# Optimization experiments

Measured on AMD Instinct MI355X. Metric: run time of the kernel, lower is better.

The kernel has to match this reference:

```python
import jax, jax.numpy as jnp
import numpy as np

# Model dims: batch, seq, d_model, heads, layers, vocab, ffn, max_distance
B, S, D, H, L, V, F, M = 2, 1024, 1024, 16, 6, 32000, 4096, 1024
Dh = D // H


def setup_inputs() -> dict:
    key = jax.random.key(0)
    ks = jax.random.split(key, 24)
    std = 0.02
    w = lambda k, shape: (jax.random.normal(k, shape, jnp.float32) * std)
    return {
        "tokens": jax.random.randint(ks[0], (B, S), 0, V, jnp.int32),
        "emb": w(ks[1], (V, D)),
        "Wq": w(ks[2], (L, D, D)), "bq": jnp.zeros((L, D), jnp.float32),
        "Wk": w(ks[3], (L, D, D)), "bk": jnp.zeros((L, D), jnp.float32),
        "Wv": w(ks[4], (L, D, D)), "bv": jnp.zeros((L, D), jnp.float32),
        "Wo": w(ks[5], (L, D, D)), "bo": jnp.zeros((L, D), jnp.float32),
        "rpe": w(ks[6], (L, M, Dh)),  # per-layer key-RPE embedding table
        "ln1_s": jnp.ones((L, D), jnp.float32), "ln1_b": jnp.zeros((L, D), jnp.float32),
        "ln2_s": jnp.ones((L, D), jnp.float32), "ln2_b": jnp.zeros((L, D), jnp.float32),
        "W1": w(ks[7], (L, D, F)), "b1": jnp.zeros((L, F), jnp.float32),
        "W2": w(ks[8], (L, F, D)), "b2": jnp.zeros((L, D), jnp.float32),
        "Wout": w(ks[9], (D, V)), "bout": jnp.zeros((V,), jnp.float32),
    }


def _ln(x, s, b):
    mu = jnp.mean(x, -1, keepdims=True)
    var = jnp.mean((x - mu) ** 2, -1, keepdims=True)
    return (x - mu) * jax.lax.rsqrt(var + 1e-5) * s + b


def _forward(tokens, emb, Wq, bq, Wk, bk, Wv, bv, Wo, bo, rpe,
             ln1_s, ln1_b, ln2_s, ln2_b, W1, b1, W2, b2, Wout, bout):
    x = emb[tokens]  # (B, S, D); dropout is identity at inference
    mask = jnp.tril(jnp.ones((S, S), bool))
    inv_sqrt_d = np.float32(1.0 / np.sqrt(Dh))

    def block(x, p):
        (wq, bq_, wk, bk_, wv, bv_, wo, bo_, rp,
         l1s, l1b, l2s, l2b, w1, b1_, w2, b2_) = p
        heads = lambda W, b: (x @ W + b).reshape(B, S, H, Dh).transpose(0, 2, 1, 3)
        q, k, v = heads(wq, bq_), heads(wk, bk_), heads(wv, bv_)
        qk = jnp.einsum('bhqd,bhkd->bhqk', q, k)
        # Music-Transformer skew: srel = Q @ E^T, pad-left 1, reshape, drop first row
        srel = jnp.einsum('bhqd,md->bhqm', q, rp[-S:])  # M == S, no clipping branch
        srel = jnp.pad(srel, ((0, 0), (0, 0), (0, 0), (1, 0)))
        srel = srel.reshape(B, H, S + 1, S)[:, :, 1:, :]
        logits = (qk + srel) * inv_sqrt_d
        logits = jnp.where(mask, logits, jnp.float32(-1e9))
        wgt = jax.nn.softmax(logits, axis=-1)
        o = jnp.einsum('bhqk,bhkd->bhqd', wgt, v).transpose(0, 2, 1, 3).reshape(B, S, D)
        o = o @ wo + bo_
        x2 = _ln(x + o, l1s, l1b)           # post-LN residual (attention)
        f = jax.nn.gelu(x2 @ w1 + b1_) @ w2 + b2_
        return _ln(x2 + f, l2s, l2b), None  # post-LN residual (FFN)

    x, _ = jax.lax.scan(block, x, (Wq, bq, Wk, bk, Wv, bv, Wo, bo, rpe,
                                   ln1_s, ln1_b, ln2_s, ln2_b, W1, b1, W2, b2))
    return x @ Wout + bout  # (B, S, V)


def reference(tokens, emb, Wq, bq, Wk, bk, Wv, bv, Wo, bo, rpe,
              ln1_s, ln1_b, ln2_s, ln2_b, W1, b1, W2, b2, Wout, bout):
    return _forward(tokens, emb, Wq, bq, Wk, bk, Wv, bv, Wo, bo, rpe,
                    ln1_s, ln1_b, ln2_s, ln2_b, W1, b1, W2, b2, Wout, bout)
```

## Files before the change

kernel.cpp:

```cpp
#include <hip/hip_runtime.h>
#include <hip/hip_bf16.h>
#include <cstdint>

constexpr int NB = 2, NS = 1024, ND = 1024, NH = 16, NL = 6, NV = 32000, NF = 4096, NDH = 64;

using bf16 = __hip_bfloat16;
typedef __bf16 bf16x8 __attribute__((ext_vector_type(8)));
typedef float f32x4 __attribute__((ext_vector_type(4)));

#define AS1(p) ((const __attribute__((address_space(1))) void*)(p))
#define AS3(p) ((__attribute__((address_space(3))) void*)(p))

__device__ __forceinline__ float gelu_f(float x) {
  float z = 1.5957691216057308f * (x + 0.044715f * x * x * x);
  return x / (1.f + __expf(-z));
}

template<int EP, bool HASBIAS>
__global__ __launch_bounds__(256)
void gemm128_bt(const bf16* __restrict__ A, const bf16* __restrict__ Bt,
                void* __restrict__ Cv, const float* __restrict__ bias,
                int K, int lda, int ldb, int ldc, long sEP)
{
  const int nM = gridDim.y, nN = gridDim.x;
  const int nwg = nM * nN;
  const int bid = blockIdx.y * nN + blockIdx.x;
  const int qq = nwg >> 3;
  const int wg = (bid & 7) * qq + (bid >> 3);
  const int m0 = (wg % nM) * 128;
  const int n0 = (wg / nM) * 256;

  __shared__ char lds[73728];

  const int tid  = threadIdx.x;
  const int lane = tid & 63;
  const int wid  = tid >> 6;
  const int wn   = wid * 64;
  const int l15  = lane & 15;
  const int rdk  = ((lane >> 4) * 16) ^ ((l15 >> 3) << 5);

  const int srow = wid * 16 + (lane >> 2);
  const int scol = ((lane & 3) * 8) ^ (((lane >> 5) & 1) << 4);
  const bf16* gA = A  + (long)(m0 + srow) * lda + scol;
  const bf16* gB = Bt + (long)(n0 + srow) * ldb + scol;
  const long a64 = 64l * lda, b64 = 64l * ldb;

  f32x4 acc[8][4] = {};
  const int NT = K >> 5;

#define STG(t_, b_) do {                                                               \
    char* dA = lds + (b_) * 24576 + wid * 1024;                                        \
    char* dB = lds + (b_) * 24576 + 8192 + wid * 1024;                                 \
    const long ko_ = (long)(t_) * 32;                                                  \
    __builtin_amdgcn_global_load_lds(AS1(gA + ko_),           AS3(dA),         16, 0, 0); \
    __builtin_amdgcn_global_load_lds(AS1(gA + ko_ + a64),     AS3(dA + 4096),  16, 0, 0); \
    __builtin_amdgcn_global_load_lds(AS1(gB + ko_),           AS3(dB),         16, 0, 0); \
    __builtin_amdgcn_global_load_lds(AS1(gB + ko_ + b64),     AS3(dB + 4096),  16, 0, 0); \
    __builtin_amdgcn_global_load_lds(AS1(gB + ko_ + 2 * b64), AS3(dB + 8192),  16, 0, 0); \
    __builtin_amdgcn_global_load_lds(AS1(gB + ko_ + 3 * b64), AS3(dB + 12288), 16, 0, 0); \
  } while (0)

#define TBODY(cur_) do {                                                               \
    const char* la_ = lds + (cur_) * 24576;                                            \
    const char* lb_ = la_ + 8192;                                                      \
    bf16x8 bf_[4], af_[8];                                                             \
    _Pragma("unroll") for (int j_ = 0; j_ < 4; ++j_)                                   \
      bf_[j_] = *(const bf16x8*)(lb_ + (wn + j_ * 16 + l15) * 64 + rdk);               \
    _Pragma("unroll") for (int i_ = 0; i_ < 8; ++i_)                                   \
      af_[i_] = *(const bf16x8*)(la_ + (i_ * 16 + l15) * 64 + rdk);                    \
    __builtin_amdgcn_s_setprio(1);                                                     \
    _Pragma("unroll") for (int i_ = 0; i_ < 8; ++i_)                                   \
      _Pragma("unroll") for (int j_ = 0; j_ < 4; ++j_)                                 \
        acc[i_][j_] = __builtin_amdgcn_mfma_f32_16x16x32_bf16(af_[i_], bf_[j_], acc[i_][j_], 0, 0, 0); \
    __builtin_amdgcn_s_setprio(0);                                                     \
  } while (0)

  STG(0, 0); STG(1, 1);
  int cur = 0, nxt = 2;
  for (int t = 0; t < NT - 1; ++t) {
    asm volatile("s_waitcnt vmcnt(6)" ::: "memory");
    __builtin_amdgcn_s_barrier();
    asm volatile("" ::: "memory");
    if (t + 2 < NT) STG(t + 2, nxt);
    TBODY(cur);
    cur = (cur == 2) ? 0 : cur + 1;
    nxt = (nxt == 2) ? 0 : nxt + 1;
  }
  asm volatile("s_waitcnt vmcnt(0)" ::: "memory");
  __builtin_amdgcn_s_barrier();
  asm volatile("" ::: "memory");
  TBODY(cur);
#undef TBODY
#undef STG

  const int rq = (lane >> 4) * 4;
  #pragma unroll
  for (int i = 0; i < 8; ++i) {
    const int r0 = m0 + i * 16 + rq;
    #pragma unroll
    for (int j = 0; j < 4; ++j) {
      const int c = n0 + wn + j * 16 + l15;
      float bv = 0.f;
      if constexpr (HASBIAS) bv = bias[c];
      #pragma unroll
      for (int e = 0; e < 4; ++e) {
        float v = acc[i][j][e] + bv;
        if constexpr (EP == 0) {
          ((float*)Cv)[(long)(r0 + e) * ldc + c] = v;
        } else if constexpr (EP == 2) {
          ((bf16*)Cv)[(long)(r0 + e) * ldc + c] = __float2bfloat16(gelu_f(v));
        } else {
          ((bf16*)Cv)[(long)(c >> 10) * sEP + (long)(r0 + e) * ND + (c & 1023)] =
              __float2bfloat16(v);
        }
      }
    }
  }
}

template<int BN, int EP, int CZ, bool HASBIAS, int SWZ, int KS>
__global__ __launch_bounds__(256)
void gemm_bt(const bf16* __restrict__ A, const bf16* __restrict__ Bt,
             void* __restrict__ Cv, const float* __restrict__ bias,
             int M, int N, int K, int lda, int ldb, int ldc, int ZH,
             long sAb, long sAh, long sBb, long sBh, long sCb, long sCh, long sBias)
{
  constexpr int BM = 128, BK = 32;
  constexpr int WGN = (BN == 128) ? 2 : 1;
  constexpr int FM  = (BM / (4 / WGN)) / 16;
  constexpr int FN  = (BN / WGN) / 16;

  const int z  = blockIdx.z;
  const int zb = z / ZH, zh = z % ZH;
  const bf16* Ab = A + (long)zb * sAb + (long)zh * sAh;
  const bf16* Bb = Bt + (long)zb * sBb + (long)zh * sBh;

  int m0, n0;
  if constexpr (SWZ == 1) {
    const int nM = gridDim.y, nN = gridDim.x;
    const int nwg = nM * nN;
    const int bid = blockIdx.y * nN + blockIdx.x;
    const int qq = nwg >> 3;
    const int wg = (bid & 7) * qq + (bid >> 3);
    m0 = (wg % nM) * BM;
    n0 = (wg / nM) * BN;
  } else {
    m0 = blockIdx.y * BM;
    n0 = blockIdx.x * BN;
  }

  if constexpr (CZ == 3) { if (m0 + n0 + BM + BN - 2 < NS - 1) return; }

  int kLen = K;
  long kOff = 0;
  if constexpr (KS == 1) { kLen = K >> 1; kOff = (long)z * kLen; }

  __shared__ bf16 Asm[BM * BK];
  __shared__ bf16 Bsm[BN * BK];

  const int tid  = threadIdx.x;
  const int lane = tid & 63;
  const int wid  = tid >> 6;
  const int wm = (wid / WGN) * (FM * 16);
  const int wn = (wid % WGN) * (FN * 16);
  const int l15 = lane & 15;
  const int lk8 = (lane >> 4) * 8;

  f32x4 acc[FM][FN] = {};

  const int srow = tid >> 2;
  const int scol = (tid & 3) * 8;
  const bf16* gA = Ab + (long)(m0 + srow) * lda + scol + kOff;
  const bf16* gB = Bb + (long)(n0 + srow) * ldb + scol + kOff;
  bf16* ldsA = Asm + wid * 512;
  bf16* ldsB = Bsm + wid * 512;

  for (int k0 = 0; k0 < kLen; k0 += BK) {
    __builtin_amdgcn_global_load_lds(AS1(gA + k0), AS3(ldsA), 16, 0, 0);
    __builtin_amdgcn_global_load_lds(AS1(gA + 64l * lda + k0), AS3(ldsA + 2048), 16, 0, 0);
    __builtin_amdgcn_global_load_lds(AS1(gB + k0), AS3(ldsB), 16, 0, 0);
    if constexpr (BN == 128)
      __builtin_amdgcn_global_load_lds(AS1(gB + 64l * ldb + k0), AS3(ldsB + 2048), 16, 0, 0);
    asm volatile("s_waitcnt vmcnt(0)" ::: "memory");
    __syncthreads();

    bf16x8 af[FM], bfr[FN];
    #pragma unroll
    for (int i = 0; i < FM; ++i)
      af[i] = *reinterpret_cast<const bf16x8*>(&Asm[(wm + i * 16 + l15) * BK + lk8]);
    #pragma unroll
    for (int j = 0; j < FN; ++j)
      bfr[j] = *reinterpret_cast<const bf16x8*>(&Bsm[(wn + j * 16 + l15) * BK + lk8]);
    #pragma unroll
    for (int i = 0; i < FM; ++i)
      #pragma unroll
      for (int j = 0; j < FN; ++j)
        acc[i][j] = __builtin_amdgcn_mfma_f32_16x16x32_bf16(af[i], bfr[j], acc[i][j], 0, 0, 0);
    __syncthreads();
  }

  const int rq = (lane >> 4) * 4;
  const long cb = (long)zb * sCb + (long)zh * sCh;
  #pragma unroll
  for (int i = 0; i < FM; ++i) {
    const int r0 = m0 + wm + i * 16 + rq;
    #pragma unroll
    for (int j = 0; j < FN; ++j) {
      const int c = n0 + wn + j * 16 + l15;
      float bv = 0.f;
      if constexpr (HASBIAS) { if (KS == 0 || z == 0) bv = bias[(long)zb * sBias + c]; }
      #pragma unroll
      for (int e = 0; e < 4; ++e) {
        float v = acc[i][j][e] + bv;
        const long idx = cb + (long)(r0 + e) * ldc + c;
        if constexpr (EP == 0) ((float*)Cv)[idx] = v;
        else                   ((bf16*)Cv)[idx] = __float2bfloat16(v);
      }
    }
  }
}

__global__ __launch_bounds__(256)
void flash_attn_k(const bf16* __restrict__ qkv, const bf16* __restrict__ vt,
                  const bf16* __restrict__ qe, bf16* __restrict__ ob)
{
  const int z  = blockIdx.x;
  const int qt = 15 - blockIdx.y;
  const int b  = z >> 4, h = z & 15;
  const int q0 = qt * 64;
  const int tid  = threadIdx.x;
  const int lane = tid & 63;
  const int wid  = tid >> 6;
  const int l15  = lane & 15;
  const int g4   = lane >> 4;
  const int xk   = (l15 & 7) << 4;

  __shared__ char lds[58368];
  char* Qlds = lds;
  char* Klds = lds + 8192;
  char* Vlds = lds + 24576;
  char* Plds = lds + 40960;

  const bf16* Qg  = qkv + ((long)b * NS + q0) * ND + h * 64;
  const bf16* Kg  = qkv + (long)NB * NS * ND + (long)b * NS * ND + h * 64;
  const bf16* Vg  = vt + (long)z * 64 * NS;
  const bf16* QEg = qe + (long)z * NS * NS;

  #pragma unroll
  for (int i = 0; i < 2; ++i) {
    const int slot = i * 256 + tid;
    const int r = slot >> 3, seg = slot & 7;
    const int sc = (seg ^ (r & 7)) * 8;
    __builtin_amdgcn_global_load_lds(AS1(Qg + (long)r * ND + sc),
                                     AS3(Qlds + (i * 4096 + wid * 1024)), 16, 0, 0);
  }

  f32x4 aqk[8], apv[4];
  #pragma unroll
  for (int j = 0; j < 4; ++j) apv[j] = (f32x4){0.f, 0.f, 0.f, 0.f};
  float mrun[4] = {-3e38f, -3e38f, -3e38f, -3e38f};
  float lrun[4] = {0.f, 0.f, 0.f, 0.f};

  const int nk = (q0 + 191) >> 7;

  for (int kt = 0; kt < nk; ++kt) {
    const int k0 = kt * 128;
    __builtin_amdgcn_s_barrier();

    #pragma unroll
    for (int i = 0; i < 4; ++i) {
      const int slot = i * 256 + tid;
      const int r = slot >> 3, seg = slot & 7;
      const int sc = (seg ^ (r & 7)) * 8;
      __builtin_amdgcn_global_load_lds(AS1(Kg + (long)(k0 + r) * ND + sc),
                                       AS3(Klds + (i * 4096 + wid * 1024)), 16, 0, 0);
    }
    #pragma unroll
    for (int i = 0; i < 4; ++i) {
      const int slot = i * 256 + tid;
      const int d = slot >> 4, seg = slot & 15;
      const int sc = (seg ^ (d & 7)) * 8;
      __builtin_amdgcn_global_load_lds(AS1(Vg + (long)d * NS + k0 + sc),
                                       AS3(Vlds + (i * 4096 + wid * 1024)), 16, 0, 0);
    }

    unsigned short se[4][8];
    #pragma unroll
    for (int e = 0; e < 4; ++e) {
      const int qg = q0 + wid * 16 + g4 * 4 + e;
      const long rowb = (long)qg * NS;
      #pragma unroll
      for (int f = 0; f < 8; ++f) {
        int m = 1023 - qg + k0 + 16 * f + l15;
        m = m > 1023 ? 1023 : m;
        se[e][f] = *(const unsigned short*)(QEg + rowb + m);
      }
    }

    asm volatile("s_waitcnt vmcnt(0)" ::: "memory");
    __builtin_amdgcn_s_barrier();

    #pragma unroll
    for (int f = 0; f < 8; ++f) aqk[f] = (f32x4){0.f, 0.f, 0.f, 0.f};
    #pragma unroll
    for (int ds = 0; ds < 2; ++ds) {
      const int ko = (ds * 32 + g4 * 8) * 2;
      bf16x8 a = *(const bf16x8*)(Qlds + (((wid * 16 + l15) * 128 + ko) ^ xk));
      #pragma unroll
      for (int f = 0; f < 8; ++f) {
        bf16x8 bb = *(const bf16x8*)(Klds + (((16 * f + l15) * 128 + ko) ^ xk));
        aqk[f] = __builtin_amdgcn_mfma_f32_16x16x32_bf16(a, bb, aqk[f], 0, 0, 0);
      }
    }

    float ps[4][8];
    float scl[4];
    #pragma unroll
    for (int e = 0; e < 4; ++e) {
      const int qg = q0 + wid * 16 + g4 * 4 + e;
      float s[8];
      float mx = mrun[e];
      #pragma unroll
      for (int f = 0; f < 8; ++f) {
        const int kg = k0 + 16 * f + l15;
        const float sv = __uint_as_float((unsigned)se[e][f] << 16);
        const float t = (aqk[f][e] + sv) * 0.125f;
        s[f] = (kg <= qg) ? t : -1e30f;
        mx = fmaxf(mx, s[f]);
      }
      #pragma unroll
      for (int o = 1; o < 16; o <<= 1) mx = fmaxf(mx, __shfl_xor(mx, o));
      const float sc_ = __expf(mrun[e] - mx);
      float ls = 0.f;
      #pragma unroll
      for (int f = 0; f < 8; ++f) { const float p = __expf(s[f] - mx); ps[e][f] = p; ls += p; }
      #pragma unroll
      for (int o = 1; o < 16; o <<= 1) ls += __shfl_xor(ls, o);
      lrun[e] = lrun[e] * sc_ + ls;
      mrun[e] = mx;
      scl[e] = sc_;
    }
    #pragma unroll
    for (int fd = 0; fd < 4; ++fd)
      #pragma unroll
      for (int e = 0; e < 4; ++e) apv[fd][e] *= scl[e];

    #pragma unroll
    for (int e = 0; e < 4; ++e) {
      char* pr = Plds + (wid * 16 + g4 * 4 + e) * 272 + l15 * 2;
      #pragma unroll
      for (int f = 0; f < 8; ++f)
        *(bf16*)(pr + f * 32) = __float2bfloat16(ps[e][f]);
    }
    asm volatile("s_waitcnt lgkmcnt(0)" ::: "memory");
    __builtin_amdgcn_sched_barrier(0);

    #pragma unroll
    for (int ks = 0; ks < 4; ++ks) {
      const int ko = (ks * 32 + g4 * 8) * 2;
      bf16x8 a = *(const bf16x8*)(Plds + (wid * 16 + l15) * 272 + ko);
      #pragma unroll
      for (int fd = 0; fd < 4; ++fd) {
        bf16x8 bb = *(const bf16x8*)(Vlds + (((16 * fd + l15) * 256 + ko) ^ xk));
        apv[fd] = __builtin_amdgcn_mfma_f32_16x16x32_bf16(a, bb, apv[fd], 0, 0, 0);
      }
    }
  }

  #pragma unroll
  for (int e = 0; e < 4; ++e) {
    const float rl = 1.f / lrun[e];
    const int qg = q0 + wid * 16 + g4 * 4 + e;
    bf16* orow = ob + ((long)b * NS + qg) * ND + h * 64;
    #pragma unroll
    for (int fd = 0; fd < 4; ++fd)
      orow[16 * fd + l15] = __float2bfloat16(apv[fd][e] * rl);
  }
}

__global__ void transpose64_k(const float* __restrict__ in, bf16* __restrict__ out,
                              int R, int C, long inZ, long outZ) {
  __shared__ float t[64][65];
  const float* ip = in + (long)blockIdx.z * inZ;
  bf16* op = out + (long)blockIdx.z * outZ;
  const int c0 = blockIdx.x * 64, r0 = blockIdx.y * 64;
  const int tid = threadIdx.x;
  const int lr = tid >> 4;
  const int lc = (tid & 15) * 4;
  #pragma unroll
  for (int i = 0; i < 4; ++i) {
    const float4 v = *(const float4*)(ip + (long)(r0 + lr + 16 * i) * C + c0 + lc);
    t[lr + 16 * i][lc]     = v.x;
    t[lr + 16 * i][lc + 1] = v.y;
    t[lr + 16 * i][lc + 2] = v.z;
    t[lr + 16 * i][lc + 3] = v.w;
  }
  __syncthreads();
  #pragma unroll
  for (int i = 0; i < 4; ++i) {
    const int oc = lr + 16 * i;
    ushort4 u;
    bf16 h0 = __float2bfloat16(t[lc][oc]);
    bf16 h1 = __float2bfloat16(t[lc + 1][oc]);
    bf16 h2 = __float2bfloat16(t[lc + 2][oc]);
    bf16 h3 = __float2bfloat16(t[lc + 3][oc]);
    u.x = *(unsigned short*)&h0; u.y = *(unsigned short*)&h1;
    u.z = *(unsigned short*)&h2; u.w = *(unsigned short*)&h3;
    *(ushort4*)(op + (long)(c0 + oc) * R + r0 + lc) = u;
  }
}

__global__ void transpose_v_k(const bf16* __restrict__ v, bf16* __restrict__ vt) {
  __shared__ bf16 t[32][33];
  const int z = blockIdx.z, b = z >> 4, h = z & 15;
  const bf16* ip = v + (long)b * NS * ND + h * 64;
  bf16* op = vt + (long)z * 64 * NS;
  const int s0 = blockIdx.x * 32, d0 = blockIdx.y * 32;
  const int tx = threadIdx.x, ty = threadIdx.y;
  #pragma unroll
  for (int i = 0; i < 4; ++i)
    t[ty * 4 + i][tx] = ip[(long)(s0 + ty * 4 + i) * ND + d0 + tx];
  __syncthreads();
  #pragma unroll
  for (int i = 0; i < 4; ++i)
    op[(long)(d0 + ty * 4 + i) * NS + s0 + tx] = t[tx][ty * 4 + i];
}

__global__ void cvt_bf16_k(const float* __restrict__ in, bf16* __restrict__ out, int n) {
  int i = blockIdx.x * 256 + threadIdx.x;
  if (i < n) out[i] = __float2bfloat16(in[i]);
}

__global__ void pack3_k(const float* __restrict__ a, const float* __restrict__ b,
                        const float* __restrict__ c, float* __restrict__ out) {
  int i = blockIdx.x * 256 + threadIdx.x;
  if (i >= NL * 3 * ND) return;
  int d = i % ND, r = (i / ND) % 3, l = i / (3 * ND);
  const float* src = (r == 0) ? a : ((r == 1) ? b : c);
  out[i] = src[l * ND + d];
}

__global__ void embed_k(const int* __restrict__ tok, const float* __restrict__ emb,
                        float* __restrict__ x, bf16* __restrict__ xb) {
  const int row = blockIdx.x;
  const int t = tok[row];
  const float4 val = ((const float4*)(emb + (long)t * ND))[threadIdx.x];
  ((float4*)(x + (long)row * ND))[threadIdx.x] = val;
  bf16* xp = xb + (long)row * ND + threadIdx.x * 4;
  xp[0] = __float2bfloat16(val.x); xp[1] = __float2bfloat16(val.y);
  xp[2] = __float2bfloat16(val.z); xp[3] = __float2bfloat16(val.w);
}

__global__ void resid_ln_k(float* __restrict__ x, const float* __restrict__ g0,
                           const float* __restrict__ g1,
                           const float* __restrict__ s, const float* __restrict__ b,
                           bf16* __restrict__ xb) {
  const int row = blockIdx.x, tid = threadIdx.x;
  const float4 xv = ((const float4*)(x + (long)row * ND))[tid];
  const float4 ga = ((const float4*)(g0 + (long)row * ND))[tid];
  const float4 gb = ((const float4*)(g1 + (long)row * ND))[tid];
  float h0 = xv.x + ga.x + gb.x, h1 = xv.y + ga.y + gb.y;
  float h2 = xv.z + ga.z + gb.z, h3 = xv.w + ga.w + gb.w;
  float ls = h0 + h1 + h2 + h3;
  __shared__ float red[8];
  #pragma unroll
  for (int o = 32; o; o >>= 1) ls += __shfl_xor(ls, o);
  const int lane = tid & 63, wid = tid >> 6;
  if (lane == 0) red[wid] = ls;
  __syncthreads();
  const float mu = (red[0] + red[1] + red[2] + red[3]) * (1.f / ND);
  const float d0 = h0 - mu, d1 = h1 - mu, d2 = h2 - mu, d3 = h3 - mu;
  float lv = d0 * d0 + d1 * d1 + d2 * d2 + d3 * d3;
  #pragma unroll
  for (int o = 32; o; o >>= 1) lv += __shfl_xor(lv, o);
  if (lane == 0) red[4 + wid] = lv;
  __syncthreads();
  const float rs = rsqrtf((red[4] + red[5] + red[6] + red[7]) * (1.f / ND) + 1e-5f);
  const float4 sv = ((const float4*)s)[tid];
  const float4 bv = ((const float4*)b)[tid];
  const float y0 = d0 * rs * sv.x + bv.x, y1 = d1 * rs * sv.y + bv.y;
  const float y2 = d2 * rs * sv.z + bv.z, y3 = d3 * rs * sv.w + bv.w;
  ((float4*)(x + (long)row * ND))[tid] = make_float4(y0, y1, y2, y3);
  bf16* xp = xb + (long)row * ND + tid * 4;
  xp[0] = __float2bfloat16(y0); xp[1] = __float2bfloat16(y1);
  xp[2] = __float2bfloat16(y2); xp[3] = __float2bfloat16(y3);
}

extern "C" void kernel_launch(void* const* d_in, const int* in_sizes, int n_in,
                              void* d_out, int out_size, void* d_ws, size_t ws_size,
                              hipStream_t stream) {
  const int*   tokens = (const int*)d_in[0];
  const float* emb  = (const float*)d_in[1];
  const float* Wq   = (const float*)d_in[2];
  const float* bq   = (const float*)d_in[3];
  const float* Wk   = (const float*)d_in[4];
  const float* bk   = (const float*)d_in[5];
  const float* Wv   = (const float*)d_in[6];
  const float* bv   = (const float*)d_in[7];
  const float* Wo   = (const float*)d_in[8];
  const float* bo   = (const float*)d_in[9];
  const float* rpe  = (const float*)d_in[10];
  const float* ln1s = (const float*)d_in[11];
  const float* ln1b = (const float*)d_in[12];
  const float* ln2s = (const float*)d_in[13];
  const float* ln2b = (const float*)d_in[14];
  const float* W1   = (const float*)d_in[15];
  const float* b1   = (const float*)d_in[16];
  const float* W2   = (const float*)d_in[17];
  const float* b2   = (const float*)d_in[18];
  const float* Wout = (const float*)d_in[19];
  const float* bout = (const float*)d_in[20];
  float* out = (float*)d_out;

  char* wsb = (char*)d_ws;
  size_t off = 0;
  auto take = [&](size_t bytes) -> void* {
    void* r = wsb + off;
    off = (off + bytes + 255) & ~(size_t)255;
    return r;
  };
  bf16*  wqkvT = (bf16*)take((size_t)NL * 3 * ND * ND * 2);
  bf16*  woT   = (bf16*)take((size_t)NL * ND * ND * 2);
  bf16*  w1T   = (bf16*)take((size_t)NL * NF * ND * 2);
  bf16*  w2T   = (bf16*)take((size_t)NL * ND * NF * 2);
  bf16*  woutT = (bf16*)take((size_t)NV * ND * 2);
  bf16*  rpeb  = (bf16*)take((size_t)NL * NS * NDH * 2);
  float* qkvb  = (float*)take((size_t)NL * 3 * ND * 4);
  float* x     = (float*)take((size_t)NB * NS * ND * 4);
  bf16*  xb    = (bf16*)take((size_t)NB * NS * ND * 2);
  bf16*  qkv   = (bf16*)take((size_t)3 * NB * NS * ND * 2);
  bf16*  vt    = (bf16*)take((size_t)NB * NS * ND * 2);
  bf16*  ob    = (bf16*)take((size_t)NB * NS * ND * 2);
  float* g     = (float*)take((size_t)2 * NB * NS * ND * 4);
  bf16*  hbuf  = (bf16*)take((size_t)NB * NS * NF * 2);
  bf16*  qe    = (bf16*)take((size_t)NB * NH * NS * NS * 2 + 4096);
  (void)in_sizes; (void)n_in; (void)out_size; (void)ws_size;

  const long gStride = (long)NB * NS * ND;

  transpose64_k<<<dim3(ND/64, ND/64, NL), 256, 0, stream>>>(Wq, wqkvT,                   ND, ND, (long)ND*ND, (long)3*ND*ND);
  transpose64_k<<<dim3(ND/64, ND/64, NL), 256, 0, stream>>>(Wk, wqkvT + (size_t)ND*ND,   ND, ND, (long)ND*ND, (long)3*ND*ND);
  transpose64_k<<<dim3(ND/64, ND/64, NL), 256, 0, stream>>>(Wv, wqkvT + (size_t)2*ND*ND, ND, ND, (long)ND*ND, (long)3*ND*ND);
  transpose64_k<<<dim3(ND/64, ND/64, NL), 256, 0, stream>>>(Wo, woT,                     ND, ND, (long)ND*ND, (long)ND*ND);
  transpose64_k<<<dim3(NF/64, ND/64, NL), 256, 0, stream>>>(W1, w1T,                     ND, NF, (long)ND*NF, (long)NF*ND);
  transpose64_k<<<dim3(ND/64, NF/64, NL), 256, 0, stream>>>(W2, w2T,                     NF, ND, (long)NF*ND, (long)ND*NF);
  transpose64_k<<<dim3(NV/64, ND/64, 1),  256, 0, stream>>>(Wout, woutT,                 ND, NV, 0, 0);
  cvt_bf16_k<<<(NL*NS*NDH + 255)/256, 256, 0, stream>>>(rpe, rpeb, NL*NS*NDH);
  pack3_k<<<(NL*3*ND + 255)/256, 256, 0, stream>>>(bq, bk, bv, qkvb);
  embed_k<<<NB*NS, 256, 0, stream>>>(tokens, emb, x, xb);

  const dim3 tb(32, 8);
  for (int l = 0; l < NL; ++l) {
    gemm128_bt<3, true><<<dim3(3*ND/256, NB*NS/128), 256, 0, stream>>>(
        xb, wqkvT + (size_t)l*3*ND*ND, qkv, qkvb + (size_t)l*3*ND,
        ND, ND, ND, ND, gStride);
    transpose_v_k<<<dim3(NS/32, 2, NB*NH), tb, 0, stream>>>(qkv + (size_t)2*NB*NS*ND, vt);
    gemm_bt<128, 1, 3, false, 0, 0><<<dim3(NS/128, NS/128, NB*NH), 256, 0, stream>>>(
        qkv, rpeb + (size_t)l*NS*NDH, qe, nullptr,
        NS, NS, NDH, ND, NDH, NS, NH,
        (long)NS*ND, 64, 0, 0, (long)NH*NS*NS, (long)NS*NS, 0);
    flash_attn_k<<<dim3(NB*NH, 16), 256, 0, stream>>>(qkv, vt, qe, ob);
    gemm_bt<128, 0, 0, true, 1, 1><<<dim3(ND/128, NB*NS/128, 2), 256, 0, stream>>>(
        ob, woT + (size_t)l*ND*ND, g, bo + (size_t)l*ND,
        NB*NS, ND, ND, ND, ND, ND, 1, 0,0, 0,0, gStride, 0, 0);
    resid_ln_k<<<NB*NS, 256, 0, stream>>>(x, g, g + gStride,
        ln1s + (size_t)l*ND, ln1b + (size_t)l*ND, xb);
    gemm128_bt<2, true><<<dim3(NF/256, NB*NS/128), 256, 0, stream>>>(
        xb, w1T + (size_t)l*NF*ND, hbuf, b1 + (size_t)l*NF, ND, ND, ND, NF, 0);
    gemm_bt<128, 0, 0, true, 1, 1><<<dim3(ND/128, NB*NS/128, 2), 256, 0, stream>>>(
        hbuf, w2T + (size_t)l*ND*NF, g, b2 + (size_t)l*ND,
        NB*NS, ND, NF, NF, NF, ND, 1, 0,0, 0,0, gStride, 0, 0);
    resid_ln_k<<<NB*NS, 256, 0, stream>>>(x, g, g + gStride,
        ln2s + (size_t)l*ND, ln2b + (size_t)l*ND, xb);
  }
  gemm128_bt<0, true><<<dim3(NV/256, NB*NS/128), 256, 0, stream>>>(
      xb, woutT, out, bout, ND, ND, ND, NV, 0);
}
```

Before: 1.560 ms.

## Add 256x256 pipelined GEMM for vocab projection and 4-way split-K for Wo/W2

```diff
diff --git a/kernel.cpp b/kernel.cpp
--- a/kernel.cpp
+++ b/kernel.cpp
@@ -17,6 +17,129 @@
 }
 
 template<int EP, bool HASBIAS>
+__global__ __launch_bounds__(512)
+void gemm256p(const bf16* __restrict__ A, const bf16* __restrict__ Bt,
+              void* __restrict__ Cv, const float* __restrict__ bias,
+              int K, int lda, int ldb, int ldc)
+{
+  const int nM = gridDim.y, nN = gridDim.x;
+  const int nwg = nM * nN;
+  const int bid = blockIdx.y * nN + blockIdx.x;
+  const int wg = (bid & 7) * (nwg >> 3) + (bid >> 3);
+  const int m0 = (wg % nM) * 256;
+  const int n0 = (wg / nM) * 256;
+
+  __shared__ char lds[131072];
+
+  const int tid = threadIdx.x, lane = tid & 63, wid = tid >> 6;
+  const int wm = (wid >> 2) * 128;
+  const int wn = (wid & 3) * 64;
+  const int l15 = lane & 15, g4 = lane >> 4;
+  const int rdk = (g4 * 16) ^ ((l15 >> 3) << 5);
+
+  const int srow = wid * 16 + (lane >> 2);
+  const int scol = ((lane & 3) * 8) ^ (((lane >> 5) & 1) << 4);
+  const bf16* gA = A  + (long)(m0 + srow) * lda + scol;
+  const bf16* gB = Bt + (long)(n0 + srow) * ldb + scol;
+  const long a128 = 128l * lda, b128 = 128l * ldb;
+
+  f32x4 acc[8][4] = {};
+  const int NT = K >> 6;
+
+#define SGA(bufsel_, t_, kc_) do {                                                     \
+    char* d_ = lds + (bufsel_) * 65536 + (kc_) * 16384 + wid * 1024;                   \
+    const long ko_ = (long)(t_) * 64 + (kc_) * 32;                                     \
+    __builtin_amdgcn_global_load_lds(AS1(gA + ko_),        AS3(d_),        16, 0, 0);  \
+    __builtin_amdgcn_global_load_lds(AS1(gA + ko_ + a128), AS3(d_ + 8192), 16, 0, 0);  \
+  } while (0)
+#define SGB(bufsel_, t_, kc_) do {                                                     \
+    char* d_ = lds + (bufsel_) * 65536 + 32768 + (kc_) * 16384 + wid * 1024;           \
+    const long ko_ = (long)(t_) * 64 + (kc_) * 32;                                     \
+    __builtin_amdgcn_global_load_lds(AS1(gB + ko_),        AS3(d_),        16, 0, 0);  \
+    __builtin_amdgcn_global_load_lds(AS1(gB + ko_ + b128), AS3(d_ + 8192), 16, 0, 0);  \
+  } while (0)
+
+#define PH(vm_, bufsel_, kc_, ih_, RDB_, STGX_) do {                                   \
+    asm volatile("s_waitcnt vmcnt(" #vm_ ")" ::: "memory");                            \
+    __builtin_amdgcn_s_barrier();                                                      \
+    asm volatile("" ::: "memory");                                                     \
+    const char* la_ = lds + (bufsel_) * 65536 + (kc_) * 16384;                         \
+    const char* lb_ = lds + (bufsel_) * 65536 + 32768 + (kc_) * 16384;                 \
+    if (RDB_) {                                                                        \
+      _Pragma("unroll") for (int j_ = 0; j_ < 4; ++j_)                                 \
+        bfr[j_] = *(const bf16x8*)(lb_ + (wn + j_ * 16 + l15) * 64 + rdk);             \
+    }                                                                                  \
+    bf16x8 af_[4];                                                                     \
+    _Pragma("unroll") for (int i2_ = 0; i2_ < 4; ++i2_)                                \
+      af_[i2_] = *(const bf16x8*)(la_ + (wm + (ih_) * 64 + i2_ * 16 + l15) * 64 + rdk);\
+    STGX_;                                                                             \
+    __builtin_amdgcn_s_setprio(1);                                                     \
+    _Pragma("unroll") for (int i2_ = 0; i2_ < 4; ++i2_)                                \
+      _Pragma("unroll") for (int j_ = 0; j_ < 4; ++j_)                                 \
+        acc[(ih_) * 4 + i2_][j_] = __builtin_amdgcn_mfma_f32_16x16x32_bf16(            \
+            af_[i2_], bfr[j_], acc[(ih_) * 4 + i2_][j_], 0, 0, 0);                     \
+    __builtin_amdgcn_s_setprio(0);                                                     \
+    asm volatile("" ::: "memory");                                                     \
+    __builtin_amdgcn_s_barrier();                                                      \
+  } while (0)
+
+  SGB(0, 0, 0);
+  SGA(0, 0, 0);
+  SGB(0, 0, 1);
+  SGA(0, 0, 1);
+  SGB(1, 1, 0);
+  SGA(1, 1, 0);
+  SGB(1, 1, 1);
+
+  for (int i = 0; i < (NT >> 1) - 1; ++i) {
+    const int t1 = 2 * i + 1, t2 = 2 * i + 2, t3 = 2 * i + 3;
+    bf16x8 bfr[4];
+    PH(10, 0, 0, 0, 1, SGA(1, t1, 1));
+    PH(12, 0, 0, 1, 0, SGB(0, t2, 0));
+    PH(10, 0, 1, 0, 1, SGA(0, t2, 0));
+    PH(12, 0, 1, 1, 0, SGB(0, t2, 1));
+    PH(10, 1, 0, 0, 1, SGA(0, t2, 1));
+    PH(12, 1, 0, 1, 0, SGB(1, t3, 0));
+    PH(10, 1, 1, 0, 1, SGA(1, t3, 0));
+    PH(12, 1, 1, 1, 0, SGB(1, t3, 1));
+  }
+  {
+    const int t1 = NT - 1;
+    bf16x8 bfr[4];
+    PH(10, 0, 0, 0, 1, SGA(1, t1, 1));
+    PH(12, 0, 0, 1, 0, (void)0);
+    PH( 8, 0, 1, 0, 1, (void)0);
+    PH( 8, 0, 1, 1, 0, (void)0);
+    PH( 4, 1, 0, 0, 1, (void)0);
+    PH( 4, 1, 0, 1, 0, (void)0);
+    PH( 0, 1, 1, 0, 1, (void)0);
+    PH( 0, 1, 1, 1, 0, (void)0);
+  }
+#undef PH
+#undef SGA
+#undef SGB
+
+  const int rq = (lane >> 4) * 4;
+  #pragma unroll
+  for (int i = 0; i < 8; ++i) {
+    const int r0 = m0 + wm + i * 16 + rq;
+    #pragma unroll
+    for (int j = 0; j < 4; ++j) {
+      const int c = n0 + wn + j * 16 + l15;
+      float bv = 0.f;
+      if constexpr (HASBIAS) bv = bias[c];
+      #pragma unroll
+      for (int e = 0; e < 4; ++e) {
+        float v = acc[i][j][e] + bv;
+        if constexpr (EP == 2) v = gelu_f(v);
+        if constexpr (EP == 0) ((float*)Cv)[(long)(r0 + e) * ldc + c] = v;
+        else                   ((bf16*)Cv)[(long)(r0 + e) * ldc + c] = __float2bfloat16(v);
+      }
+    }
+  }
+}
+
+template<int EP, bool HASBIAS, int KSZ>
 __global__ __launch_bounds__(256)
 void gemm128_bt(const bf16* __restrict__ A, const bf16* __restrict__ Bt,
                 void* __restrict__ Cv, const float* __restrict__ bias,
@@ -30,6 +153,9 @@
   const int m0 = (wg % nM) * 128;
   const int n0 = (wg / nM) * 256;
 
+  const int kLen = K / KSZ;
+  const long kOff = (long)blockIdx.z * kLen;
+
   __shared__ char lds[73728];
 
   const int tid  = threadIdx.x;
@@ -41,12 +167,12 @@
 
   const int srow = wid * 16 + (lane >> 2);
   const int scol = ((lane & 3) * 8) ^ (((lane >> 5) & 1) << 4);
-  const bf16* gA = A  + (long)(m0 + srow) * lda + scol;
-  const bf16* gB = Bt + (long)(n0 + srow) * ldb + scol;
+  const bf16* gA = A  + (long)(m0 + srow) * lda + scol + kOff;
+  const bf16* gB = Bt + (long)(n0 + srow) * ldb + scol + kOff;
   const long a64 = 64l * lda, b64 = 64l * ldb;
 
   f32x4 acc[8][4] = {};
-  const int NT = K >> 5;
+  const int NT = kLen >> 5;
 
 #define STG(t_, b_) do {                                                               \
     char* dA = lds + (b_) * 24576 + wid * 1024;                                        \
@@ -101,12 +227,13 @@
     for (int j = 0; j < 4; ++j) {
       const int c = n0 + wn + j * 16 + l15;
       float bv = 0.f;
-      if constexpr (HASBIAS) bv = bias[c];
+      if constexpr (HASBIAS) { if (KSZ == 1 || blockIdx.z == 0) bv = bias[c]; }
       #pragma unroll
       for (int e = 0; e < 4; ++e) {
         float v = acc[i][j][e] + bv;
         if constexpr (EP == 0) {
-          ((float*)Cv)[(long)(r0 + e) * ldc + c] = v;
+          float* Cz = (float*)Cv + (KSZ > 1 ? (long)blockIdx.z * sEP : 0);
+          Cz[(long)(r0 + e) * ldc + c] = v;
         } else if constexpr (EP == 2) {
           ((bf16*)Cv)[(long)(r0 + e) * ldc + c] = __float2bfloat16(gelu_f(v));
         } else {
@@ -135,25 +262,10 @@
   const bf16* Ab = A + (long)zb * sAb + (long)zh * sAh;
   const bf16* Bb = Bt + (long)zb * sBb + (long)zh * sBh;
 
-  int m0, n0;
-  if constexpr (SWZ == 1) {
-    const int nM = gridDim.y, nN = gridDim.x;
-    const int nwg = nM * nN;
-    const int bid = blockIdx.y * nN + blockIdx.x;
-    const int qq = nwg >> 3;
-    const int wg = (bid & 7) * qq + (bid >> 3);
-    m0 = (wg % nM) * BM;
-    n0 = (wg / nM) * BN;
-  } else {
-    m0 = blockIdx.y * BM;
-    n0 = blockIdx.x * BN;
-  }
+  const int m0 = blockIdx.y * BM;
+  const int n0 = blockIdx.x * BN;
 
   if constexpr (CZ == 3) { if (m0 + n0 + BM + BN - 2 < NS - 1) return; }
-
-  int kLen = K;
-  long kOff = 0;
-  if constexpr (KS == 1) { kLen = K >> 1; kOff = (long)z * kLen; }
 
   __shared__ bf16 Asm[BM * BK];
   __shared__ bf16 Bsm[BN * BK];
@@ -170,12 +282,12 @@
 
   const int srow = tid >> 2;
   const int scol = (tid & 3) * 8;
-  const bf16* gA = Ab + (long)(m0 + srow) * lda + scol + kOff;
-  const bf16* gB = Bb + (long)(n0 + srow) * ldb + scol + kOff;
+  const bf16* gA = Ab + (long)(m0 + srow) * lda + scol;
+  const bf16* gB = Bb + (long)(n0 + srow) * ldb + scol;
   bf16* ldsA = Asm + wid * 512;
   bf16* ldsB = Bsm + wid * 512;
 
-  for (int k0 = 0; k0 < kLen; k0 += BK) {
+  for (int k0 = 0; k0 < K; k0 += BK) {
     __builtin_amdgcn_global_load_lds(AS1(gA + k0), AS3(ldsA), 16, 0, 0);
     __builtin_amdgcn_global_load_lds(AS1(gA + 64l * lda + k0), AS3(ldsA + 2048), 16, 0, 0);
     __builtin_amdgcn_global_load_lds(AS1(gB + k0), AS3(ldsB), 16, 0, 0);
@@ -208,7 +320,7 @@
     for (int j = 0; j < FN; ++j) {
       const int c = n0 + wn + j * 16 + l15;
       float bv = 0.f;
-      if constexpr (HASBIAS) { if (KS == 0 || z == 0) bv = bias[(long)zb * sBias + c]; }
+      if constexpr (HASBIAS) bv = bias[(long)zb * sBias + c];
       #pragma unroll
       for (int e = 0; e < 4; ++e) {
         float v = acc[i][j][e] + bv;
@@ -451,16 +563,20 @@
   xp[2] = __float2bfloat16(val.z); xp[3] = __float2bfloat16(val.w);
 }
 
-__global__ void resid_ln_k(float* __restrict__ x, const float* __restrict__ g0,
-                           const float* __restrict__ g1,
+__global__ void resid_ln_k(float* __restrict__ x, const float* __restrict__ g,
+                           long gs,
                            const float* __restrict__ s, const float* __restrict__ b,
                            bf16* __restrict__ xb) {
   const int row = blockIdx.x, tid = threadIdx.x;
   const float4 xv = ((const float4*)(x + (long)row * ND))[tid];
-  const float4 ga = ((const float4*)(g0 + (long)row * ND))[tid];
-  const float4 gb = ((const float4*)(g1 + (long)row * ND))[tid];
-  float h0 = xv.x + ga.x + gb.x, h1 = xv.y + ga.y + gb.y;
-  float h2 = xv.z + ga.z + gb.z, h3 = xv.w + ga.w + gb.w;
+  const float4 ga = ((const float4*)(g + (long)row * ND))[tid];
+  const float4 gb = ((const float4*)(g + gs + (long)row * ND))[tid];
+  const float4 gc = ((const float4*)(g + 2 * gs + (long)row * ND))[tid];
+  const float4 gd = ((const float4*)(g + 3 * gs + (long)row * ND))[tid];
+  float h0 = xv.x + ga.x + gb.x + gc.x + gd.x;
+  float h1 = xv.y + ga.y + gb.y + gc.y + gd.y;
+  float h2 = xv.z + ga.z + gb.z + gc.z + gd.z;
+  float h3 = xv.w + ga.w + gb.w + gc.w + gd.w;
   float ls = h0 + h1 + h2 + h3;
   __shared__ float red[8];
   #pragma unroll
@@ -531,7 +647,7 @@
   bf16*  qkv   = (bf16*)take((size_t)3 * NB * NS * ND * 2);
   bf16*  vt    = (bf16*)take((size_t)NB * NS * ND * 2);
   bf16*  ob    = (bf16*)take((size_t)NB * NS * ND * 2);
-  float* g     = (float*)take((size_t)2 * NB * NS * ND * 4);
+  float* g     = (float*)take((size_t)4 * NB * NS * ND * 4);
   bf16*  hbuf  = (bf16*)take((size_t)NB * NS * NF * 2);
   bf16*  qe    = (bf16*)take((size_t)NB * NH * NS * NS * 2 + 4096);
   (void)in_sizes; (void)n_in; (void)out_size; (void)ws_size;
@@ -551,7 +667,7 @@
 
   const dim3 tb(32, 8);
   for (int l = 0; l < NL; ++l) {
-    gemm128_bt<3, true><<<dim3(3*ND/256, NB*NS/128), 256, 0, stream>>>(
+    gemm128_bt<3, true, 1><<<dim3(3*ND/256, NB*NS/128), 256, 0, stream>>>(
         xb, wqkvT + (size_t)l*3*ND*ND, qkv, qkvb + (size_t)l*3*ND,
         ND, ND, ND, ND, gStride);
     transpose_v_k<<<dim3(NS/32, 2, NB*NH), tb, 0, stream>>>(qkv + (size_t)2*NB*NS*ND, vt);
@@ -560,19 +676,17 @@
         NS, NS, NDH, ND, NDH, NS, NH,
         (long)NS*ND, 64, 0, 0, (long)NH*NS*NS, (long)NS*NS, 0);
     flash_attn_k<<<dim3(NB*NH, 16), 256, 0, stream>>>(qkv, vt, qe, ob);
-    gemm_bt<128, 0, 0, true, 1, 1><<<dim3(ND/128, NB*NS/128, 2), 256, 0, stream>>>(
-        ob, woT + (size_t)l*ND*ND, g, bo + (size_t)l*ND,
-        NB*NS, ND, ND, ND, ND, ND, 1, 0,0, 0,0, gStride, 0, 0);
-    resid_ln_k<<<NB*NS, 256, 0, stream>>>(x, g, g + gStride,
+    gemm128_bt<0, true, 4><<<dim3(ND/256, NB*NS/128, 4), 256, 0, stream>>>(
+        ob, woT + (size_t)l*ND*ND, g, bo + (size_t)l*ND, ND, ND, ND, ND, gStride);
+    resid_ln_k<<<NB*NS, 256, 0, stream>>>(x, g, gStride,
         ln1s + (size_t)l*ND, ln1b + (size_t)l*ND, xb);
-    gemm128_bt<2, true><<<dim3(NF/256, NB*NS/128), 256, 0, stream>>>(
+    gemm128_bt<2, true, 1><<<dim3(NF/256, NB*NS/128), 256, 0, stream>>>(
         xb, w1T + (size_t)l*NF*ND, hbuf, b1 + (size_t)l*NF, ND, ND, ND, NF, 0);
-    gemm_bt<128, 0, 0, true, 1, 1><<<dim3(ND/128, NB*NS/128, 2), 256, 0, stream>>>(
-        hbuf, w2T + (size_t)l*ND*NF, g, b2 + (size_t)l*ND,
-        NB*NS, ND, NF, NF, NF, ND, 1, 0,0, 0,0, gStride, 0, 0);
-    resid_ln_k<<<NB*NS, 256, 0, stream>>>(x, g, g + gStride,
+    gemm128_bt<0, true, 4><<<dim3(ND/256, NB*NS/128, 4), 256, 0, stream>>>(
+        hbuf, w2T + (size_t)l*ND*NF, g, b2 + (size_t)l*ND, NF, NF, NF, ND, gStride);
+    resid_ln_k<<<NB*NS, 256, 0, stream>>>(x, g, gStride,
         ln2s + (size_t)l*ND, ln2b + (size_t)l*ND, xb);
   }
-  gemm128_bt<0, true><<<dim3(NV/256, NB*NS/128), 256, 0, stream>>>(
-      xb, woutT, out, bout, ND, ND, ND, NV, 0);
-}
+  gemm256p<0, true><<<dim3(NV/256, NB*NS/256), 512, 0, stream>>>(
+      xb, woutT, out, bout, ND, ND, ND, NV);
+}
```

Measured after the change: 1.358 ms. -13.0%, faster.
